# Kernel optimization log

Hardware: AMD Instinct MI355X
Metric: run time of the kernel (lower is better)

Reference implementation:

```python
import jax, jax.numpy as jnp
import numpy as np

N, E, H, HEADS, T = 40000, 320000, 128, 4, 3
DH = H // HEADS


def setup_inputs() -> dict:
    key = jax.random.key(0)
    ks = jax.random.split(key, 32)
    f32 = jnp.float32

    def w(k, shape, s=0.05):
        return (s * jax.random.normal(k, shape)).astype(f32)

    inp = {
        "x": jax.random.normal(ks[0], (N, H), dtype=f32),
        "edge_index": jax.random.randint(ks[1], (2, E), 0, N, dtype=jnp.int32),
        "edge_attr": 0.1 * jax.random.normal(ks[2], (E, H), dtype=f32),
        "wq": w(ks[3], (H, H)), "bq": w(ks[4], (H,)),
        "wk": w(ks[5], (H, H)), "bk": w(ks[6], (H,)),
        "wv": w(ks[7], (H, H)), "bv": w(ks[8], (H,)),
        "w_ao": w(ks[9], (H, H)), "b_ao": w(ks[10], (H,)),
        "ln1_g": jnp.ones((H,), f32), "ln1_b": jnp.zeros((H,), f32),
        "w_int": w(ks[11], (4 * H, H)), "b_int": w(ks[12], (4 * H,)),
        "w_out": w(ks[13], (H, 4 * H)), "b_out": w(ks[14], (H,)),
        "ln2_g": jnp.ones((H,), f32), "ln2_b": jnp.zeros((H,), f32),
        "w_ih": w(ks[15], (3 * H, H)), "w_hh": w(ks[16], (3 * H, H)),
        "b_ih": w(ks[17], (3 * H,)), "b_hh": w(ks[18], (3 * H,)),
        "ln3_g": jnp.ones((H,), f32), "ln3_b": jnp.zeros((H,), f32),
    }
    return inp


def _ln(x, g, b, eps=1e-12):
    u = jnp.mean(x, axis=-1, keepdims=True)
    s = jnp.mean((x - u) ** 2, axis=-1, keepdims=True)
    return g * (x - u) / jnp.sqrt(s + eps) + b


def _gat(x, src, dst, edge_attr, wq, bq, wk, bk, wv, bv):
    # per-edge gather: x_i = target features, x_j = source features (+ pseudo)
    x_i = x[dst]                       # [E, H]
    x_j = x[src] + edge_attr           # [E, H]
    q = (x_i @ wq.T + bq).reshape(-1, HEADS, DH)
    k = (x_j @ wk.T + bk).reshape(-1, HEADS, DH)
    v = (x_j @ wv.T + bv).reshape(-1, HEADS, DH)
    alpha = jnp.sum(q * k, axis=-1) / jnp.sqrt(jnp.float32(DH))  # [E, HEADS]
    # segment softmax over incoming edges of each target node
    m = jax.ops.segment_max(alpha, dst, num_segments=N)
    m = jnp.where(jnp.isfinite(m), m, jnp.zeros_like(m))
    a = jnp.exp(alpha - m[dst])
    s = jax.ops.segment_sum(a, dst, num_segments=N)
    a = a / (s[dst] + 1e-16)
    out = jax.ops.segment_sum(a[..., None] * v, dst, num_segments=N)  # [N, HEADS, DH]
    return out.reshape(N, H)


def reference(x, edge_index, edge_attr, wq, bq, wk, bk, wv, bv,
              w_ao, b_ao, ln1_g, ln1_b, w_int, b_int, w_out, b_out,
              ln2_g, ln2_b, w_ih, w_hh, b_ih, b_hh, ln3_g, ln3_b):
    src, dst = edge_index[0], edge_index[1]
    h = x  # GRU hidden state, [N, H] (seq_len=1, batch=N)
    for _ in range(T):
        att = _gat(x, src, dst, edge_attr, wq, bq, wk, bk, wv, bv)
        att = _ln(att @ w_ao.T + b_ao + x, ln1_g, ln1_b)
        inter = jax.nn.gelu(att @ w_int.T + b_int, approximate=False)
        m = _ln(inter @ w_out.T + b_out + att, ln2_g, ln2_b)
        # single-step GRU (torch gate order: r, z, n)
        gi = m @ w_ih.T + b_ih
        gh = h @ w_hh.T + b_hh
        ir, iz, inn = jnp.split(gi, 3, axis=-1)
        hr, hz, hn = jnp.split(gh, 3, axis=-1)
        r = jax.nn.sigmoid(ir + hr)
        z = jax.nn.sigmoid(iz + hz)
        n = jnp.tanh(inn + r * hn)
        h = (1.0 - z) * n + z * h
        x = _ln(h, ln3_g, ln3_b)
    return x
```

## Files before the change

kernel.cpp:

```cpp
#include <hip/hip_runtime.h>
#include <hip/hip_bf16.h>
#include <math.h>

#define N_NODES 40000
#define N_EDGES 320000
#define T_ITERS 3

typedef __attribute__((ext_vector_type(8))) short short8;
typedef __attribute__((ext_vector_type(4))) short short4v;
typedef __attribute__((ext_vector_type(4))) float f32x4;

static __device__ __forceinline__ short f2bf(float f) {
    union { float f; unsigned u; } x; x.f = f;
    unsigned r = (x.u + 0x7fffu + ((x.u >> 16) & 1u)) >> 16;
    return (short)r;
}
static __device__ __forceinline__ float bf2f(short s) {
    union { unsigned u; float f; } x; x.u = ((unsigned)(unsigned short)s) << 16;
    return x.f;
}

template<int NI>
__global__ __launch_bounds__(256) void gemm_bf16(
    const short* __restrict__ A, const short* __restrict__ W,
    const float* __restrict__ bias, short* __restrict__ Cb,
    int M, int K, int NC)
{
    constexpr int NT = 32 * NI;
    __shared__ __align__(16) short As[64 * 40];
    __shared__ __align__(16) short Ws[NT * 40];

    const int tid  = threadIdx.x;
    const int lane = tid & 63, wid = tid >> 6;
    const int wm = wid & 1, wn = wid >> 1;
    const int t16 = lane & 15, quad = lane >> 4;
    const long blockM = (long)blockIdx.x * 64;
    const int colBase = blockIdx.y * NT;

    f32x4 acc[2][NI];
    for (int i = 0; i < 2; i++)
        for (int j = 0; j < NI; j++)
            acc[i][j] = (f32x4){0.f, 0.f, 0.f, 0.f};

    for (int k0 = 0; k0 < K; k0 += 32) {
        {
            const int r = tid >> 2, c = (tid & 3) * 8;
            *(short8*)&As[r * 40 + c] = *(const short8*)(A + (blockM + r) * K + k0 + c);
        }
        for (int gg = 0; gg < NI / 2; gg++) {
            const int chunk = tid + gg * 256;
            const int r = chunk >> 2, c = (chunk & 3) * 8;
            *(short8*)&Ws[r * 40 + c] =
                *(const short8*)(W + (long)(colBase + r) * K + k0 + c);
        }
        __syncthreads();
        short8 a0 = *(const short8*)&As[(wm * 32 + t16) * 40 + quad * 8];
        short8 a1 = *(const short8*)&As[(wm * 32 + 16 + t16) * 40 + quad * 8];
        for (int ni = 0; ni < NI; ni++) {
            short8 bf = *(const short8*)&Ws[(wn * 16 * NI + ni * 16 + t16) * 40 + quad * 8];
            acc[0][ni] = __builtin_amdgcn_mfma_f32_16x16x32_bf16(a0, bf, acc[0][ni], 0, 0, 0);
            acc[1][ni] = __builtin_amdgcn_mfma_f32_16x16x32_bf16(a1, bf, acc[1][ni], 0, 0, 0);
        }
        __syncthreads();
    }

    for (int mi = 0; mi < 2; mi++)
        for (int ni = 0; ni < NI; ni++) {
            const int gc = colBase + wn * 16 * NI + ni * 16 + t16;
            for (int r = 0; r < 4; r++) {
                long gr = blockM + wm * 32 + mi * 16 + quad * 4 + r;
                float v = acc[mi][ni][r];
                if (bias) v += bias[gc];
                Cb[gr * (long)NC + gc] = f2bf(v);
            }
        }
}

__global__ __launch_bounds__(256) void ekv_kernel(
    const float* __restrict__ ea, const short* __restrict__ Wkv,
    const float* __restrict__ bkv, short* __restrict__ EKV)
{
    __shared__ __align__(16) char smem[64 * 276 * 2];
    short* As = (short*)smem;
    short* Ws = (short*)(smem + 64 * 40 * 2);
    short* Cs = (short*)smem;

    const int tid  = threadIdx.x;
    const int lane = tid & 63, wid = tid >> 6;
    const int t16 = lane & 15, quad = lane >> 4;
    const long blockM = (long)blockIdx.x * 64;

    f32x4 acc[4][4];
    for (int i = 0; i < 4; i++)
        for (int j = 0; j < 4; j++)
            acc[i][j] = (f32x4){0.f, 0.f, 0.f, 0.f};

    for (int k0 = 0; k0 < 128; k0 += 32) {
        for (int g = 0; g < 2; g++) {
            const int r = (tid >> 3) + g * 32, c = (tid & 7) * 4;
            const float4 v = *(const float4*)(ea + (blockM + r) * 128 + k0 + c);
            short4v sv;
            sv.x = f2bf(v.x); sv.y = f2bf(v.y); sv.z = f2bf(v.z); sv.w = f2bf(v.w);
            *(short4v*)&As[r * 40 + c] = sv;
        }
        for (int g = 0; g < 4; g++) {
            const int idx = tid + g * 256;
            const int r = idx >> 2, c = (idx & 3) * 8;
            *(short8*)&Ws[r * 40 + c] = *(const short8*)(Wkv + (long)r * 128 + k0 + c);
        }
        __syncthreads();
        short8 a[4];
        for (int mi = 0; mi < 4; mi++)
            a[mi] = *(const short8*)&As[(mi * 16 + t16) * 40 + quad * 8];
        for (int ni = 0; ni < 4; ni++) {
            short8 bf = *(const short8*)&Ws[(wid * 64 + ni * 16 + t16) * 40 + quad * 8];
            for (int mi = 0; mi < 4; mi++)
                acc[mi][ni] = __builtin_amdgcn_mfma_f32_16x16x32_bf16(a[mi], bf, acc[mi][ni], 0, 0, 0);
        }
        __syncthreads();
    }

    for (int mi = 0; mi < 4; mi++)
        for (int ni = 0; ni < 4; ni++) {
            const int col = wid * 64 + ni * 16 + t16;
            const float bv_ = bkv[col];
            for (int r = 0; r < 4; r++) {
                const int row = mi * 16 + quad * 4 + r;
                Cs[row * 276 + col] = f2bf(acc[mi][ni][r] + bv_);
            }
        }
    __syncthreads();
    for (int it = 0; it < 8; it++) {
        const int idx = it * 256 + tid;
        const int row = idx >> 5, c8 = idx & 31;
        *(short8*)(EKV + (blockM + row) * 256 + c8 * 8) = *(const short8*)&Cs[row * 276 + c8 * 8];
    }
}

__global__ __launch_bounds__(256) void edge_attn_kernel(
    const short* __restrict__ QKVb, const short* __restrict__ EKV,
    const int* __restrict__ rowptr, const int2* __restrict__ epair,
    short* __restrict__ outb)
{
    const int wid = threadIdx.x >> 6, lane = threadIdx.x & 63;
    const int n = blockIdx.x * 4 + wid;
    if (n >= N_NODES) return;
    const int g = lane >> 3, l8 = lane & 7;
    const int d0 = l8 * 16;
    const float scale = 0.17677669529663687f;

    short8 q0 = *(const short8*)&QKVb[(long)n * 384 + d0];
    short8 q1 = *(const short8*)&QKVb[(long)n * 384 + d0 + 8];
    float qf[16];
#pragma unroll
    for (int j = 0; j < 8; j++) { qf[j] = bf2f(q0[j]); qf[8 + j] = bf2f(q1[j]); }

    const int beg = rowptr[n], end = rowptr[n + 1];
    float acc[16];
#pragma unroll
    for (int j = 0; j < 16; j++) acc[j] = 0.f;
    float ssum = 0.f;

    for (int i0 = beg; i0 < end; i0 += 8) {
        const int i = i0 + g;
        const bool valid = i < end;
        const int ii = valid ? i : beg;
        const int2 pe = epair[ii];
        const long s = pe.x, e = pe.y;
        short8 k0 = *(const short8*)&EKV[e * 256 + d0];
        short8 k1 = *(const short8*)&EKV[e * 256 + d0 + 8];
        short8 xk0 = *(const short8*)&QKVb[s * 384 + 128 + d0];
        short8 xk1 = *(const short8*)&QKVb[s * 384 + 128 + d0 + 8];
        short8 v0 = *(const short8*)&EKV[e * 256 + 128 + d0];
        short8 v1 = *(const short8*)&EKV[e * 256 + 128 + d0 + 8];
        short8 xv0 = *(const short8*)&QKVb[s * 384 + 256 + d0];
        short8 xv1 = *(const short8*)&QKVb[s * 384 + 256 + d0 + 8];
        float dot = 0.f;
#pragma unroll
        for (int j = 0; j < 8; j++) {
            dot += qf[j] * (bf2f(k0[j]) + bf2f(xk0[j]));
            dot += qf[8 + j] * (bf2f(k1[j]) + bf2f(xk1[j]));
        }
        dot += __shfl_xor(dot, 1);
        float a = valid ? __expf(dot * scale) : 0.f;
        ssum += a;
#pragma unroll
        for (int j = 0; j < 8; j++) {
            acc[j]     += a * (bf2f(v0[j]) + bf2f(xv0[j]));
            acc[8 + j] += a * (bf2f(v1[j]) + bf2f(xv1[j]));
        }
    }
#pragma unroll
    for (int o = 8; o < 64; o <<= 1) {
#pragma unroll
        for (int j = 0; j < 16; j++) acc[j] += __shfl_xor(acc[j], o);
        ssum += __shfl_xor(ssum, o);
    }
    if (g == 0) {
        float inv = 1.0f / (ssum + 1e-16f);
        short8 o0, o1;
#pragma unroll
        for (int j = 0; j < 8; j++) { o0[j] = f2bf(acc[j] * inv); o1[j] = f2bf(acc[8 + j] * inv); }
        *(short8*)&outb[(long)n * 128 + d0] = o0;
        *(short8*)&outb[(long)n * 128 + d0 + 8] = o1;
    }
}

__global__ __launch_bounds__(256) void ffn_kernel(
    const short* __restrict__ attraw, const short* __restrict__ x,
    const short* __restrict__ Wao, const short* __restrict__ Wint,
    const short* __restrict__ Wout, const float* __restrict__ b_ao,
    const float* __restrict__ b_int, const float* __restrict__ b_out,
    const float* __restrict__ ln1_g, const float* __restrict__ ln1_b,
    const float* __restrict__ ln2_g, const float* __restrict__ ln2_b,
    short* __restrict__ Mout)
{
    __shared__ __align__(16) short As[64 * 136];
    __shared__ __align__(16) short Is[64 * 136];
    __shared__ __align__(16) short Ws[128 * 40];

    const int tid  = threadIdx.x;
    const int lane = tid & 63, wid = tid >> 6;
    const int t16 = lane & 15, quad = lane >> 4;
    const long blockM = (long)blockIdx.x * 64;

    {
        const int r = tid >> 2, c = (tid & 3) * 32;
        const long gr = blockM + r;
        for (int j = 0; j < 4; j++) {
            *(short8*)&As[r * 136 + c + j * 8] = *(const short8*)(x + gr * 128 + c + j * 8);
            *(short8*)&Is[r * 136 + c + j * 8] = *(const short8*)(attraw + gr * 128 + c + j * 8);
        }
    }
    __syncthreads();

    f32x4 acc0[8];
    for (int j = 0; j < 8; j++) acc0[j] = (f32x4){0.f, 0.f, 0.f, 0.f};
    for (int k0 = 0; k0 < 128; k0 += 32) {
        const int r = tid >> 1, c = (tid & 1) * 16;
        *(short8*)&Ws[r * 40 + c]     = *(const short8*)(Wao + (long)r * 128 + k0 + c);
        *(short8*)&Ws[r * 40 + c + 8] = *(const short8*)(Wao + (long)r * 128 + k0 + c + 8);
        __syncthreads();
        short8 a = *(const short8*)&Is[(wid * 16 + t16) * 136 + k0 + quad * 8];
        for (int ni = 0; ni < 8; ni++) {
            short8 bf = *(const short8*)&Ws[(ni * 16 + t16) * 40 + quad * 8];
            acc0[ni] = __builtin_amdgcn_mfma_f32_16x16x32_bf16(a, bf, acc0[ni], 0, 0, 0);
        }
        __syncthreads();
    }
    for (int r = 0; r < 4; r++) {
        const int row = wid * 16 + quad * 4 + r;
        float vals[8];
        float s = 0.f;
        for (int ni = 0; ni < 8; ni++) {
            const int col = ni * 16 + t16;
            float v = acc0[ni][r] + b_ao[col] + bf2f(As[row * 136 + col]);
            vals[ni] = v;
            s += v;
        }
        for (int o = 1; o < 16; o <<= 1) s += __shfl_xor(s, o);
        float u = s * (1.0f / 128.0f);
        float vs = 0.f;
        for (int ni = 0; ni < 8; ni++) { float d = vals[ni] - u; vals[ni] = d; vs += d * d; }
        for (int o = 1; o < 16; o <<= 1) vs += __shfl_xor(vs, o);
        float rstd = rsqrtf(vs * (1.0f / 128.0f) + 1e-12f);
        for (int ni = 0; ni < 8; ni++) {
            const int col = ni * 16 + t16;
            As[row * 136 + col] = f2bf(ln1_g[col] * vals[ni] * rstd + ln1_b[col]);
        }
    }
    __syncthreads();

    f32x4 acc2[8];
    for (int j = 0; j < 8; j++) acc2[j] = (f32x4){0.f, 0.f, 0.f, 0.f};
    for (int kc = 0; kc < 4; kc++) {
        f32x4 acc1[8];
        for (int j = 0; j < 8; j++) acc1[j] = (f32x4){0.f, 0.f, 0.f, 0.f};
        for (int k0 = 0; k0 < 128; k0 += 32) {
            const int r = tid >> 1, c = (tid & 1) * 16;
            *(short8*)&Ws[r * 40 + c] =
                *(const short8*)(Wint + (long)(kc * 128 + r) * 128 + k0 + c);
            *(short8*)&Ws[r * 40 + c + 8] =
                *(const short8*)(Wint + (long)(kc * 128 + r) * 128 + k0 + c + 8);
            __syncthreads();
            short8 a = *(const short8*)&As[(wid * 16 + t16) * 136 + k0 + quad * 8];
            for (int ni = 0; ni < 8; ni++) {
                short8 bf = *(const short8*)&Ws[(ni * 16 + t16) * 40 + quad * 8];
                acc1[ni] = __builtin_amdgcn_mfma_f32_16x16x32_bf16(a, bf, acc1[ni], 0, 0, 0);
            }
            __syncthreads();
        }
        for (int ni = 0; ni < 8; ni++) {
            const int col = ni * 16 + t16;
            const float bi = b_int[kc * 128 + col];
            for (int r = 0; r < 4; r++) {
                const int row = wid * 16 + quad * 4 + r;
                float v = acc1[ni][r] + bi;
                v = 0.5f * v * (1.0f + erff(v * 0.70710678118654752f));
                Is[row * 136 + col] = f2bf(v);
            }
        }
        __syncthreads();
        for (int k0 = 0; k0 < 128; k0 += 32) {
            const int r = tid >> 1, c = (tid & 1) * 16;
            *(short8*)&Ws[r * 40 + c] =
                *(const short8*)(Wout + (long)r * 512 + kc * 128 + k0 + c);
            *(short8*)&Ws[r * 40 + c + 8] =
                *(const short8*)(Wout + (long)r * 512 + kc * 128 + k0 + c + 8);
            __syncthreads();
            short8 a = *(const short8*)&Is[(wid * 16 + t16) * 136 + k0 + quad * 8];
            for (int ni = 0; ni < 8; ni++) {
                short8 bf = *(const short8*)&Ws[(ni * 16 + t16) * 40 + quad * 8];
                acc2[ni] = __builtin_amdgcn_mfma_f32_16x16x32_bf16(a, bf, acc2[ni], 0, 0, 0);
            }
            __syncthreads();
        }
    }

    for (int r = 0; r < 4; r++) {
        const int row = wid * 16 + quad * 4 + r;
        const long gr = blockM + row;
        float vals[8];
        float s = 0.f;
        for (int ni = 0; ni < 8; ni++) {
            const int col = ni * 16 + t16;
            float v = acc2[ni][r] + b_out[col] + bf2f(As[row * 136 + col]);
            vals[ni] = v;
            s += v;
        }
        for (int o = 1; o < 16; o <<= 1) s += __shfl_xor(s, o);
        float u = s * (1.0f / 128.0f);
        float vs = 0.f;
        for (int ni = 0; ni < 8; ni++) { float d = vals[ni] - u; vals[ni] = d; vs += d * d; }
        for (int o = 1; o < 16; o <<= 1) vs += __shfl_xor(vs, o);
        float rstd = rsqrtf(vs * (1.0f / 128.0f) + 1e-12f);
        for (int ni = 0; ni < 8; ni++) {
            const int col = ni * 16 + t16;
            Mout[gr * 128 + col] = f2bf(ln2_g[col] * vals[ni] * rstd + ln2_b[col]);
        }
    }
}

template<bool FINAL>
__global__ __launch_bounds__(256) void gru_kernel(
    const short* __restrict__ m, const short* __restrict__ h,
    const short* __restrict__ Wg, const float* __restrict__ bg,
    const float* __restrict__ g3, const float* __restrict__ b3,
    short* __restrict__ hout, void* __restrict__ xout)
{
    __shared__ __align__(16) char smem[64 * 520 * 2];
    short* As = (short*)smem;
    short* Ws = (short*)(smem + 64 * 40 * 2);
    short* Os = (short*)smem;

    const int tid  = threadIdx.x;
    const int lane = tid & 63, wid = tid >> 6;
    const int t16 = lane & 15, quad = lane >> 4;
    const long blockM = (long)blockIdx.x * 64;

    f32x4 acc[4][8];
    for (int i = 0; i < 4; i++)
        for (int j = 0; j < 8; j++)
            acc[i][j] = (f32x4){0.f, 0.f, 0.f, 0.f};

    for (int k0 = 0; k0 < 256; k0 += 32) {
        const short* src = (k0 < 128) ? m : h;
        {
            const int r = tid >> 2, c = (tid & 3) * 8;
            *(short8*)&As[r * 40 + c] =
                *(const short8*)(src + (blockM + r) * 128 + (k0 & 127) + c);
        }
        for (int g = 0; g < 8; g++) {
            const int idx = tid + g * 256;
            const int r = idx >> 2, c = (idx & 3) * 8;
            *(short8*)&Ws[r * 40 + c] = *(const short8*)(Wg + (long)r * 256 + k0 + c);
        }
        __syncthreads();
        short8 a[4];
        for (int mi = 0; mi < 4; mi++)
            a[mi] = *(const short8*)&As[(mi * 16 + t16) * 40 + quad * 8];
        for (int ni = 0; ni < 8; ni++) {
            short8 bf = *(const short8*)&Ws[(wid * 128 + ni * 16 + t16) * 40 + quad * 8];
            for (int mi = 0; mi < 4; mi++)
                acc[mi][ni] = __builtin_amdgcn_mfma_f32_16x16x32_bf16(a[mi], bf, acc[mi][ni], 0, 0, 0);
        }
        __syncthreads();
    }

    for (int mi = 0; mi < 4; mi++)
        for (int ni = 0; ni < 8; ni++) {
            const int col = wid * 128 + ni * 16 + t16;
            const float bb = bg[col];
            for (int r = 0; r < 4; r++) {
                const int row = mi * 16 + quad * 4 + r;
                Os[row * 520 + col] = f2bf(acc[mi][ni][r] + bb);
            }
        }
    __syncthreads();

    {
        const int row = tid >> 2;
        const int c0 = (tid & 3) * 32;
        const long gr = blockM + row;
        float hv[32];
        for (int j = 0; j < 4; j++) {
            short8 hpv = *(const short8*)(h + gr * 128 + c0 + j * 8);
            short8 orv = *(const short8*)&Os[row * 520 + c0 + j * 8];
            short8 ozv = *(const short8*)&Os[row * 520 + 128 + c0 + j * 8];
            short8 onv = *(const short8*)&Os[row * 520 + 256 + c0 + j * 8];
            short8 ohv = *(const short8*)&Os[row * 520 + 384 + c0 + j * 8];
            for (int q = 0; q < 8; q++) {
                float rr = 1.f / (1.f + __expf(-bf2f(orv[q])));
                float zz = 1.f / (1.f + __expf(-bf2f(ozv[q])));
                float nn = tanhf(bf2f(onv[q]) + rr * bf2f(ohv[q]));
                float hpq = bf2f(hpv[q]);
                hv[j * 8 + q] = (1.f - zz) * nn + zz * hpq;
            }
        }
        float s = 0.f;
        for (int j = 0; j < 32; j++) s += hv[j];
        s += __shfl_xor(s, 1); s += __shfl_xor(s, 2);
        float u = s * (1.0f / 128.0f);
        float vs = 0.f;
        for (int j = 0; j < 32; j++) { float d = hv[j] - u; vs += d * d; }
        vs += __shfl_xor(vs, 1); vs += __shfl_xor(vs, 2);
        float rstd = rsqrtf(vs * (1.0f / 128.0f) + 1e-12f);
        for (int j = 0; j < 4; j++) {
            short8 o;
            for (int q = 0; q < 8; q++) o[q] = f2bf(hv[j * 8 + q]);
            *(short8*)(hout + gr * 128 + c0 + j * 8) = o;
        }
        if (FINAL) {
            float* xo = (float*)xout;
            for (int j = 0; j < 8; j++) {
                float4 o;
                o.x = g3[c0 + j * 4 + 0] * (hv[j * 4 + 0] - u) * rstd + b3[c0 + j * 4 + 0];
                o.y = g3[c0 + j * 4 + 1] * (hv[j * 4 + 1] - u) * rstd + b3[c0 + j * 4 + 1];
                o.z = g3[c0 + j * 4 + 2] * (hv[j * 4 + 2] - u) * rstd + b3[c0 + j * 4 + 2];
                o.w = g3[c0 + j * 4 + 3] * (hv[j * 4 + 3] - u) * rstd + b3[c0 + j * 4 + 3];
                *(float4*)&xo[gr * 128 + c0 + j * 4] = o;
            }
        } else {
            short* xo = (short*)xout;
            for (int j = 0; j < 4; j++) {
                short8 o;
                for (int q = 0; q < 8; q++) {
                    const int c = c0 + j * 8 + q;
                    o[q] = f2bf(g3[c] * (hv[j * 8 + q] - u) * rstd + b3[c]);
                }
                *(short8*)(xo + gr * 128 + c0 + j * 8) = o;
            }
        }
    }
}

__global__ void count_kernel(const int* __restrict__ dst, int* __restrict__ cnt) {
    int e = blockIdx.x * 256 + threadIdx.x;
    if (e < N_EDGES) atomicAdd(&cnt[dst[e]], 1);
}

__global__ __launch_bounds__(1024) void scan_kernel(const int* __restrict__ cnt,
                                                    int* __restrict__ rowptr) {
    __shared__ int lds[1024];
    const int tid = threadIdx.x;
    const int CH = 40;
    const int base = tid * CH;
    int sum = 0;
    for (int j = 0; j < CH; j++) { int i = base + j; if (i < N_NODES) sum += cnt[i]; }
    lds[tid] = sum;
    __syncthreads();
    for (int off = 1; off < 1024; off <<= 1) {
        int v = (tid >= off) ? lds[tid - off] : 0;
        __syncthreads();
        lds[tid] += v;
        __syncthreads();
    }
    int run = lds[tid] - sum;
    for (int j = 0; j < CH; j++) {
        int i = base + j;
        if (i < N_NODES) { rowptr[i] = run; run += cnt[i]; }
    }
    if (tid == 1023) rowptr[N_NODES] = lds[1023];
}

__global__ void fill_kernel(const int* __restrict__ src, const int* __restrict__ dst,
                            const int* __restrict__ rowptr, int* __restrict__ wo,
                            int2* __restrict__ epair) {
    int e = blockIdx.x * 256 + threadIdx.x;
    if (e < N_EDGES) {
        int d = dst[e];
        int pos = atomicAdd(&wo[d], 1);
        int slot = rowptr[d] + pos;
        epair[slot] = make_int2(src[e], e);
    }
}

__global__ void cvt_kernel(const float* __restrict__ s, short* __restrict__ d, int n) {
    int i = (blockIdx.x * 256 + threadIdx.x) * 4;
    if (i < n) {
        float4 v = *(const float4*)(s + i);
        short4v sv;
        sv.x = f2bf(v.x); sv.y = f2bf(v.y); sv.z = f2bf(v.z); sv.w = f2bf(v.w);
        *(short4v*)(d + i) = sv;
    }
}
__global__ void bias_cat_kernel(const float* __restrict__ bq, const float* __restrict__ bk,
                                const float* __restrict__ bv, float* __restrict__ bqkv,
                                float* __restrict__ bkv) {
    int i = blockIdx.x * 256 + threadIdx.x;
    if (i < 384) bqkv[i] = (i < 128) ? bq[i] : 0.0f;
    if (i < 256) bkv[i] = (i < 128) ? bk[i] : bv[i - 128];
}
__global__ void build_wg_kernel(const float* __restrict__ wih, const float* __restrict__ whh,
                                const float* __restrict__ bih, const float* __restrict__ bhh,
                                short* __restrict__ Wg, float* __restrict__ bg) {
    int idx = blockIdx.x * 256 + threadIdx.x;
    if (idx < 512 * 256) {
        int r = idx >> 8, k = idx & 255;
        float v;
        if (r < 256)      v = (k < 128) ? wih[r * 128 + k] : whh[r * 128 + k - 128];
        else if (r < 384) v = (k < 128) ? wih[r * 128 + k] : 0.f;
        else              v = (k < 128) ? 0.f : whh[(r - 128) * 128 + k - 128];
        Wg[idx] = f2bf(v);
    }
    if (idx < 512) {
        float b;
        if (idx < 256)      b = bih[idx] + bhh[idx];
        else if (idx < 384) b = bih[idx];
        else                b = bhh[idx - 128];
        bg[idx] = b;
    }
}

extern "C" void kernel_launch(void* const* d_in, const int* in_sizes, int n_in,
                              void* d_out, int out_size, void* d_ws, size_t ws_size,
                              hipStream_t stream) {
    const float* x_in  = (const float*)d_in[0];
    const int*   eidx  = (const int*)d_in[1];
    const float* ea    = (const float*)d_in[2];
    const float* wq    = (const float*)d_in[3];
    const float* bq    = (const float*)d_in[4];
    const float* wk    = (const float*)d_in[5];
    const float* bk    = (const float*)d_in[6];
    const float* wv    = (const float*)d_in[7];
    const float* bv    = (const float*)d_in[8];
    const float* w_ao  = (const float*)d_in[9];
    const float* b_ao  = (const float*)d_in[10];
    const float* ln1_g = (const float*)d_in[11];
    const float* ln1_b = (const float*)d_in[12];
    const float* w_int = (const float*)d_in[13];
    const float* b_int = (const float*)d_in[14];
    const float* w_out = (const float*)d_in[15];
    const float* b_out = (const float*)d_in[16];
    const float* ln2_g = (const float*)d_in[17];
    const float* ln2_b = (const float*)d_in[18];
    const float* w_ih  = (const float*)d_in[19];
    const float* w_hh  = (const float*)d_in[20];
    const float* b_ih  = (const float*)d_in[21];
    const float* b_hh  = (const float*)d_in[22];
    const float* ln3_g = (const float*)d_in[23];
    const float* ln3_b = (const float*)d_in[24];
    const int* srcv = eidx;
    const int* dstv = eidx + N_EDGES;

    char* ws = (char*)d_ws;
    size_t off = 0;
    auto alloc = [&](size_t bytes) -> void* {
        void* p = ws + off;
        off += (bytes + 255) & ~(size_t)255;
        return p;
    };
    short* EKV  = (short*)alloc((size_t)N_EDGES * 256 * 2);
    short* Wcat = (short*)alloc(384 * 128 * 2);
    short* Wao  = (short*)alloc(128 * 128 * 2);
    short* Wint = (short*)alloc(512 * 128 * 2);
    short* Wout = (short*)alloc(128 * 512 * 2);
    short* Wg   = (short*)alloc(512 * 256 * 2);
    float* bqkv = (float*)alloc(384 * 4);
    float* bkv  = (float*)alloc(256 * 4);
    float* bg   = (float*)alloc(512 * 4);
    int* cnt    = (int*)alloc((size_t)N_NODES * 4);
    int* wo     = (int*)alloc((size_t)N_NODES * 4);
    int* rowptr = (int*)alloc((size_t)(N_NODES + 1) * 4);
    int2* epair = (int2*)alloc((size_t)N_EDGES * 8);
    short* xb     = (short*)alloc((size_t)N_NODES * 128 * 2);
    short* QKVb   = (short*)alloc((size_t)N_NODES * 384 * 2);
    short* attraw = (short*)alloc((size_t)N_NODES * 128 * 2);
    short* mbuf   = (short*)alloc((size_t)N_NODES * 128 * 2);
    short* hbuf   = (short*)alloc((size_t)N_NODES * 128 * 2);
    short* xbuf   = (short*)alloc((size_t)N_NODES * 128 * 2);
    if (off > ws_size) return;

    cvt_kernel<<<16, 256, 0, stream>>>(wq, Wcat, 16384);
    cvt_kernel<<<16, 256, 0, stream>>>(wk, Wcat + 16384, 16384);
    cvt_kernel<<<16, 256, 0, stream>>>(wv, Wcat + 32768, 16384);
    cvt_kernel<<<16, 256, 0, stream>>>(w_ao, Wao, 16384);
    cvt_kernel<<<64, 256, 0, stream>>>(w_int, Wint, 65536);
    cvt_kernel<<<64, 256, 0, stream>>>(w_out, Wout, 65536);
    cvt_kernel<<<5000, 256, 0, stream>>>(x_in, xb, N_NODES * 128);
    bias_cat_kernel<<<2, 256, 0, stream>>>(bq, bk, bv, bqkv, bkv);
    build_wg_kernel<<<512, 256, 0, stream>>>(w_ih, w_hh, b_ih, b_hh, Wg, bg);

    hipMemsetAsync(cnt, 0, (size_t)N_NODES * 4, stream);
    hipMemsetAsync(wo, 0, (size_t)N_NODES * 4, stream);
    count_kernel<<<1250, 256, 0, stream>>>(dstv, cnt);
    scan_kernel<<<1, 1024, 0, stream>>>(cnt, rowptr);
    fill_kernel<<<1250, 256, 0, stream>>>(srcv, dstv, rowptr, wo, epair);

    ekv_kernel<<<5000, 256, 0, stream>>>(ea, Wcat + 128 * 128, bkv, EKV);

    const short* xcur = xb;
    const short* hcur = xb;
    for (int t = 0; t < T_ITERS; t++) {
        gemm_bf16<4><<<dim3(625, 3), 256, 0, stream>>>(
            xcur, Wcat, bqkv, QKVb, N_NODES, 128, 384);
        edge_attn_kernel<<<10000, 256, 0, stream>>>(QKVb, EKV, rowptr, epair, attraw);
        ffn_kernel<<<625, 256, 0, stream>>>(
            attraw, xcur, Wao, Wint, Wout, b_ao, b_int, b_out,
            ln1_g, ln1_b, ln2_g, ln2_b, mbuf);
        if (t == T_ITERS - 1)
            gru_kernel<true><<<625, 256, 0, stream>>>(
                mbuf, hcur, Wg, bg, ln3_g, ln3_b, hbuf, d_out);
        else
            gru_kernel<false><<<625, 256, 0, stream>>>(
                mbuf, hcur, Wg, bg, ln3_g, ln3_b, hbuf, xbuf);
        xcur = xbuf;
        hcur = hbuf;
    }
}
```

Baseline: 1.119 ms.

## Scatter edge K/V rows into CSR order so attention reads them contiguously

The edge K/V projection now writes each edge's output row to its CSR slot, computed in the fill kernel. The attention kernel then reads EKV sequentially by slot instead of gathering by the original edge id, and needs only a source index array instead of an int2 pair. The ekv kernel also stages the whole 64x128 edge_attr tile into LDS once instead of per K step, and adds an occupancy hint. The cost is a scattered write in the one-time projection, paid once against three coalesced reads in the attention iterations.

```diff
diff --git a/kernel.cpp b/kernel.cpp
--- a/kernel.cpp
+++ b/kernel.cpp
@@ -76,13 +76,14 @@
         }
 }
 
-__global__ __launch_bounds__(256) void ekv_kernel(
+__global__ __launch_bounds__(256, 4) void ekv_kernel(
     const float* __restrict__ ea, const short* __restrict__ Wkv,
-    const float* __restrict__ bkv, short* __restrict__ EKV)
+    const float* __restrict__ bkv, const int* __restrict__ eslot,
+    short* __restrict__ EKV)
 {
-    __shared__ __align__(16) char smem[64 * 276 * 2];
+    __shared__ __align__(16) char smem[64 * 136 * 2 + 256 * 40 * 2];
     short* As = (short*)smem;
-    short* Ws = (short*)(smem + 64 * 40 * 2);
+    short* Ws = (short*)(smem + 64 * 136 * 2);
     short* Cs = (short*)smem;
 
     const int tid  = threadIdx.x;
@@ -90,19 +91,30 @@
     const int t16 = lane & 15, quad = lane >> 4;
     const long blockM = (long)blockIdx.x * 64;
 
+    {
+        const int r = tid >> 2, c0 = (tid & 3) * 32;
+        const float* gp = ea + (blockM + r) * 128 + c0;
+        for (int half = 0; half < 2; half++) {
+            float4 v0 = *(const float4*)(gp + half * 16);
+            float4 v1 = *(const float4*)(gp + half * 16 + 4);
+            float4 v2 = *(const float4*)(gp + half * 16 + 8);
+            float4 v3 = *(const float4*)(gp + half * 16 + 12);
+            short8 s0, s1;
+            s0[0] = f2bf(v0.x); s0[1] = f2bf(v0.y); s0[2] = f2bf(v0.z); s0[3] = f2bf(v0.w);
+            s0[4] = f2bf(v1.x); s0[5] = f2bf(v1.y); s0[6] = f2bf(v1.z); s0[7] = f2bf(v1.w);
+            s1[0] = f2bf(v2.x); s1[1] = f2bf(v2.y); s1[2] = f2bf(v2.z); s1[3] = f2bf(v2.w);
+            s1[4] = f2bf(v3.x); s1[5] = f2bf(v3.y); s1[6] = f2bf(v3.z); s1[7] = f2bf(v3.w);
+            *(short8*)&As[r * 136 + c0 + half * 16]     = s0;
+            *(short8*)&As[r * 136 + c0 + half * 16 + 8] = s1;
+        }
+    }
+
     f32x4 acc[4][4];
     for (int i = 0; i < 4; i++)
         for (int j = 0; j < 4; j++)
             acc[i][j] = (f32x4){0.f, 0.f, 0.f, 0.f};
 
     for (int k0 = 0; k0 < 128; k0 += 32) {
-        for (int g = 0; g < 2; g++) {
-            const int r = (tid >> 3) + g * 32, c = (tid & 7) * 4;
-            const float4 v = *(const float4*)(ea + (blockM + r) * 128 + k0 + c);
-            short4v sv;
-            sv.x = f2bf(v.x); sv.y = f2bf(v.y); sv.z = f2bf(v.z); sv.w = f2bf(v.w);
-            *(short4v*)&As[r * 40 + c] = sv;
-        }
         for (int g = 0; g < 4; g++) {
             const int idx = tid + g * 256;
             const int r = idx >> 2, c = (idx & 3) * 8;
@@ -111,7 +123,7 @@
         __syncthreads();
         short8 a[4];
         for (int mi = 0; mi < 4; mi++)
-            a[mi] = *(const short8*)&As[(mi * 16 + t16) * 40 + quad * 8];
+            a[mi] = *(const short8*)&As[(mi * 16 + t16) * 136 + k0 + quad * 8];
         for (int ni = 0; ni < 4; ni++) {
             short8 bf = *(const short8*)&Ws[(wid * 64 + ni * 16 + t16) * 40 + quad * 8];
             for (int mi = 0; mi < 4; mi++)
@@ -133,13 +145,14 @@
     for (int it = 0; it < 8; it++) {
         const int idx = it * 256 + tid;
         const int row = idx >> 5, c8 = idx & 31;
-        *(short8*)(EKV + (blockM + row) * 256 + c8 * 8) = *(const short8*)&Cs[row * 276 + c8 * 8];
+        const long orow = eslot[blockM + row];
+        *(short8*)(EKV + orow * 256 + c8 * 8) = *(const short8*)&Cs[row * 276 + c8 * 8];
     }
 }
 
 __global__ __launch_bounds__(256) void edge_attn_kernel(
     const short* __restrict__ QKVb, const short* __restrict__ EKV,
-    const int* __restrict__ rowptr, const int2* __restrict__ epair,
+    const int* __restrict__ rowptr, const int* __restrict__ esrc,
     short* __restrict__ outb)
 {
     const int wid = threadIdx.x >> 6, lane = threadIdx.x & 63;
@@ -164,15 +177,14 @@
     for (int i0 = beg; i0 < end; i0 += 8) {
         const int i = i0 + g;
         const bool valid = i < end;
-        const int ii = valid ? i : beg;
-        const int2 pe = epair[ii];
-        const long s = pe.x, e = pe.y;
-        short8 k0 = *(const short8*)&EKV[e * 256 + d0];
-        short8 k1 = *(const short8*)&EKV[e * 256 + d0 + 8];
+        const long ii = valid ? i : beg;
+        const long s = esrc[ii];
+        short8 k0 = *(const short8*)&EKV[ii * 256 + d0];
+        short8 k1 = *(const short8*)&EKV[ii * 256 + d0 + 8];
         short8 xk0 = *(const short8*)&QKVb[s * 384 + 128 + d0];
         short8 xk1 = *(const short8*)&QKVb[s * 384 + 128 + d0 + 8];
-        short8 v0 = *(const short8*)&EKV[e * 256 + 128 + d0];
-        short8 v1 = *(const short8*)&EKV[e * 256 + 128 + d0 + 8];
+        short8 v0 = *(const short8*)&EKV[ii * 256 + 128 + d0];
+        short8 v1 = *(const short8*)&EKV[ii * 256 + 128 + d0 + 8];
         short8 xv0 = *(const short8*)&QKVb[s * 384 + 256 + d0];
         short8 xv1 = *(const short8*)&QKVb[s * 384 + 256 + d0 + 8];
         float dot = 0.f;
@@ -485,13 +497,14 @@
 
 __global__ void fill_kernel(const int* __restrict__ src, const int* __restrict__ dst,
                             const int* __restrict__ rowptr, int* __restrict__ wo,
-                            int2* __restrict__ epair) {
+                            int* __restrict__ esrc, int* __restrict__ eslot) {
     int e = blockIdx.x * 256 + threadIdx.x;
     if (e < N_EDGES) {
         int d = dst[e];
         int pos = atomicAdd(&wo[d], 1);
         int slot = rowptr[d] + pos;
-        epair[slot] = make_int2(src[e], e);
+        esrc[slot] = src[e];
+        eslot[e] = slot;
     }
 }
 
@@ -582,7 +595,8 @@
     int* cnt    = (int*)alloc((size_t)N_NODES * 4);
     int* wo     = (int*)alloc((size_t)N_NODES * 4);
     int* rowptr = (int*)alloc((size_t)(N_NODES + 1) * 4);
-    int2* epair = (int2*)alloc((size_t)N_EDGES * 8);
+    int* esrc   = (int*)alloc((size_t)N_EDGES * 4);
+    int* eslot  = (int*)alloc((size_t)N_EDGES * 4);
     short* xb     = (short*)alloc((size_t)N_NODES * 128 * 2);
     short* QKVb   = (short*)alloc((size_t)N_NODES * 384 * 2);
     short* attraw = (short*)alloc((size_t)N_NODES * 128 * 2);
@@ -605,16 +619,16 @@
     hipMemsetAsync(wo, 0, (size_t)N_NODES * 4, stream);
     count_kernel<<<1250, 256, 0, stream>>>(dstv, cnt);
     scan_kernel<<<1, 1024, 0, stream>>>(cnt, rowptr);
-    fill_kernel<<<1250, 256, 0, stream>>>(srcv, dstv, rowptr, wo, epair);
-
-    ekv_kernel<<<5000, 256, 0, stream>>>(ea, Wcat + 128 * 128, bkv, EKV);
+    fill_kernel<<<1250, 256, 0, stream>>>(srcv, dstv, rowptr, wo, esrc, eslot);
+
+    ekv_kernel<<<5000, 256, 0, stream>>>(ea, Wcat + 128 * 128, bkv, eslot, EKV);
 
     const short* xcur = xb;
     const short* hcur = xb;
     for (int t = 0; t < T_ITERS; t++) {
         gemm_bf16<4><<<dim3(625, 3), 256, 0, stream>>>(
             xcur, Wcat, bqkv, QKVb, N_NODES, 128, 384);
-        edge_attn_kernel<<<10000, 256, 0, stream>>>(QKVb, EKV, rowptr, epair, attraw);
+        edge_attn_kernel<<<10000, 256, 0, stream>>>(QKVb, EKV, rowptr, esrc, attraw);
         ffn_kernel<<<625, 256, 0, stream>>>(
             attraw, xcur, Wao, Wint, Wout, b_ao, b_int, b_out,
             ln1_g, ln1_b, ln2_g, ln2_b, mbuf);
```

Result: faster. 1.072 ms (-4.1%).
